# Optimization experiments

Measured on AMD Instinct MI355X. Metric: run time of the kernel, lower is better.

Reference implementation:

```python
import jax, jax.numpy as jnp
import numpy as np
import math

B, T, C = 4, 2048, 1024
N_HEAD = 16


def setup_inputs() -> dict:
    key = jax.random.key(0)
    k1, k2, k3 = jax.random.split(key, 3)
    x = jax.random.normal(k1, (B, T, C), dtype=jnp.float32)
    W_attn = jax.random.normal(k2, (C, 3 * C), dtype=jnp.float32) * (1.0 / math.sqrt(C))
    b_attn = jnp.zeros((3 * C,), dtype=jnp.float32)
    W_proj = jax.random.normal(k3, (C, C), dtype=jnp.float32) * (1.0 / math.sqrt(C))
    b_proj = jnp.zeros((C,), dtype=jnp.float32)
    return {"x": x, "W_attn": W_attn, "b_attn": b_attn, "W_proj": W_proj, "b_proj": b_proj}


def reference(x, W_attn, b_attn, W_proj, b_proj):
    b, t, c = x.shape
    hs = c // N_HEAD  # head size
    qkv = x @ W_attn + b_attn  # [B,T,3C]
    q, k, v = jnp.split(qkv, 3, axis=-1)
    # [B,T,C] -> [B,H,T,hs]
    q = q.reshape(b, t, N_HEAD, hs).transpose(0, 2, 1, 3)
    k = k.reshape(b, t, N_HEAD, hs).transpose(0, 2, 1, 3)
    v = v.reshape(b, t, N_HEAD, hs).transpose(0, 2, 1, 3)
    att = jnp.einsum('bhqd,bhkd->bhqk', q, k) / math.sqrt(hs)  # [B,H,T,T]
    causal = jnp.tril(jnp.ones((t, t), dtype=bool))
    att = jnp.where(causal[None, None, :, :], att, -jnp.inf)
    att = jax.nn.softmax(att, axis=-1)
    y = jnp.einsum('bhqk,bhkd->bhqd', att, v)  # [B,H,T,hs]
    y = y.transpose(0, 2, 1, 3).reshape(b, t, c)
    return y @ W_proj + b_proj
```

## Files before the change

### kernel.cpp

```cpp
#include <hip/hip_runtime.h>


typedef __bf16 bf16_t;
typedef __bf16 bf16x8 __attribute__((ext_vector_type(8)));
typedef __bf16 bf16x4 __attribute__((ext_vector_type(4)));
typedef float  f32x4  __attribute__((ext_vector_type(4)));

#define MFMA16(a, b, c) __builtin_amdgcn_mfma_f32_16x16x32_bf16((a), (b), (c), 0, 0, 0)

static __device__ __forceinline__ void gld_lds16(const bf16_t* g, void* l) {
  __builtin_amdgcn_global_load_lds(
      (const __attribute__((address_space(1))) void*)(const void*)g,
      (__attribute__((address_space(3))) void*)l, 16, 0, 0);
}

static __device__ __forceinline__ bf16x8 ldv8(const void* p) {
  return *reinterpret_cast<const bf16x8*>(p);
}

static __device__ __forceinline__ float exp2_hw(float x) {
  float r;
  asm("v_exp_f32 %0, %1" : "=v"(r) : "v"(x));
  return r;
}

__global__ __launch_bounds__(256) void cvt_f32_bf16(const float* __restrict__ in,
                                                    bf16_t* __restrict__ out, int n4) {
  int i = blockIdx.x * 256 + threadIdx.x;
  if (i < n4) {
    float4 v = reinterpret_cast<const float4*>(in)[i];
    bf16x4 o;
    o[0] = (bf16_t)v.x; o[1] = (bf16_t)v.y; o[2] = (bf16_t)v.z; o[3] = (bf16_t)v.w;
    reinterpret_cast<bf16x4*>(out)[i] = o;
  }
}

__global__ __launch_bounds__(256) void transpose_cvt(const float* __restrict__ in,
                                                     bf16_t* __restrict__ out,
                                                     int Kd, int Nd) {
  __shared__ float tile[32][33];
  int tx = threadIdx.x, ty = threadIdx.y;
  int n0 = blockIdx.x * 32, k0 = blockIdx.y * 32;
#pragma unroll
  for (int i = 0; i < 4; ++i)
    tile[ty + i * 8][tx] = in[(size_t)(k0 + ty + i * 8) * Nd + (n0 + tx)];
  __syncthreads();
#pragma unroll
  for (int i = 0; i < 4; ++i)
    out[(size_t)(n0 + ty + i * 8) * Kd + (k0 + tx)] = (bf16_t)tile[tx][ty + i * 8];
}

template <int MODE>
__global__ __launch_bounds__(256) void gemm_bf16(
    const bf16_t* __restrict__ A, const bf16_t* __restrict__ Bt,
    const float* __restrict__ bias, int M, int N, int K,
    bf16_t* __restrict__ Qo, bf16_t* __restrict__ Ko, bf16_t* __restrict__ Vt,
    float* __restrict__ Co) {
  __shared__ alignas(16) char lds[32768];

  const int tid = threadIdx.x;
  const int wave = tid >> 6, lane = tid & 63;
  const int wm = wave >> 1, wn = wave & 1;
  const int l16 = lane & 15, kb = lane >> 4;

  const int nbx = gridDim.x;
  const int lb = blockIdx.y * nbx + blockIdx.x;
  const int c = lb & 7;
  const int ii = lb >> 3;
  const int rPer = gridDim.y >> 3;
  const int tmt = c * rPer + (ii % rPer);
  const int tnt = ii / rPer;
  const int tm0 = tmt * 128, tn0 = tnt * 128;

  const int srow = wave * 8 + (lane >> 3);
  const int sp = lane & 7;

  f32x4 acc[4][4] = {};

  for (int k0 = 0; k0 < K; k0 += 64) {
    __syncthreads();
#pragma unroll
    for (int inst = 0; inst < 4; ++inst) {
      const int row = inst * 32 + srow;
      const int chunk = (sp ^ (row & 7)) * 8;
      gld_lds16(A + (size_t)(tm0 + row) * K + k0 + chunk,
                &lds[inst * 4096 + wave * 1024]);
      gld_lds16(Bt + (size_t)(tn0 + row) * K + k0 + chunk,
                &lds[16384 + inst * 4096 + wave * 1024]);
    }
    __syncthreads();
#pragma unroll
    for (int kc = 0; kc < 2; ++kc) {
      bf16x8 af[4], bfr[4];
#pragma unroll
      for (int mi = 0; mi < 4; ++mi) {
        const int row = wm * 64 + mi * 16 + l16;
        const int slot = (kc * 4 + kb) ^ (row & 7);
        af[mi] = ldv8(&lds[row * 128 + slot * 16]);
      }
#pragma unroll
      for (int ni = 0; ni < 4; ++ni) {
        const int row = wn * 64 + ni * 16 + l16;
        const int slot = (kc * 4 + kb) ^ (row & 7);
        bfr[ni] = ldv8(&lds[16384 + row * 128 + slot * 16]);
      }
#pragma unroll
      for (int mi = 0; mi < 4; ++mi)
#pragma unroll
        for (int ni = 0; ni < 4; ++ni)
          acc[mi][ni] = MFMA16(af[mi], bfr[ni], acc[mi][ni]);
    }
  }

#pragma unroll
  for (int ni = 0; ni < 4; ++ni) {
    const int n = tn0 + wn * 64 + ni * 16 + l16;
    const float bv = bias[n];
#pragma unroll
    for (int mi = 0; mi < 4; ++mi) {
#pragma unroll
      for (int j = 0; j < 4; ++j) {
        const int m = tm0 + wm * 64 + mi * 16 + kb * 4 + j;
        const float v = acc[mi][ni][j] + bv;
        if constexpr (MODE == 0) {
          const int which = n >> 10, hn = n & 1023;
          const int h = hn >> 6, d = hn & 63;
          const int b = m >> 11, t = m & 2047;
          const size_t bh = (size_t)(b * 16 + h);
          if (which == 0)
            Qo[(bh * 2048 + t) * 64 + d] = (bf16_t)(v * 0.18033688011112042f);
          else if (which == 1)
            Ko[(bh * 2048 + t) * 64 + d] = (bf16_t)v;
          else
            Vt[(bh * 64 + d) * 2048 + t] = (bf16_t)v;
        } else {
          Co[(size_t)m * N + n] = v;
        }
      }
    }
  }
}

__global__ __launch_bounds__(256) void attn_fwd(const bf16_t* __restrict__ Qg,
                                                const bf16_t* __restrict__ Kg,
                                                const bf16_t* __restrict__ Vtg,
                                                bf16_t* __restrict__ Yg) {
  __shared__ alignas(16) char lds[40960];

  const int tid = threadIdx.x;
  const int wave = tid >> 6, lane = tid & 63;
  const int l16 = lane & 15, kb = lane >> 4;
  const int l8 = l16 & 7;
  const float NEG_INF = -__builtin_inff();

  const int n = blockIdx.x;
  const int bh = (n & 7) * 8 + ((n >> 3) & 7);
  const int qt = 31 - (n >> 6);
  const size_t base = (size_t)bh * (2048 * 64);
  const int b = bh >> 4, h = bh & 15;

  const int srow = tid >> 3;
  const int schunk = (tid & 7) ^ (srow & 7);
  const bf16_t* Ksrc = Kg + base + (size_t)srow * 64 + schunk * 8;
  const bf16_t* Vsrc = Vtg + base + (size_t)srow * 2048 + schunk * 8;

  auto stageK = [&](int buf, int kv0) {
    char* kd = lds + buf * 8192 + wave * 1024;
    const bf16_t* ks = Ksrc + (size_t)kv0 * 64;
    gld_lds16(ks, kd);
    gld_lds16(ks + 2048, kd + 4096);
  };
  auto stageV = [&](int buf, int kv0) {
    char* vd = lds + 16384 + buf * 8192 + wave * 1024;
    const bf16_t* vs = Vsrc + kv0;
    gld_lds16(vs, vd);
    gld_lds16(vs + 65536, vd + 4096);
  };

  const int q0 = qt * 64 + wave * 16;
  const int q = q0 + l16;
  const int trips = qt + 1;

  const bf16x8 qf0 = ldv8(Qg + base + (size_t)q * 64 + kb * 8);
  const bf16x8 qf1 = ldv8(Qg + base + (size_t)q * 64 + 32 + kb * 8);

  f32x4 o[4] = {};
  float m_r = NEG_INF, l_r = 0.f;

  char* Pw = lds + 32768 + wave * 2048;

  stageK(0, 0);
  stageV(0, 0);
  asm volatile("s_waitcnt vmcnt(0)" ::: "memory");
  __builtin_amdgcn_s_barrier();
  __builtin_amdgcn_sched_barrier(0);

  int cur = 0;
  for (int t = 0; t < trips; ++t) {
    const int kv0 = t * 64;
    const bool more = (t + 1 < trips);
    if (more) {
      stageK(cur ^ 1, kv0 + 64);
      stageV(cur ^ 1, kv0 + 64);
    }

    const char* Kb = lds + cur * 8192;
    const char* Vb = lds + 16384 + cur * 8192;

    bf16x8 kf[8];
#pragma unroll
    for (int i = 0; i < 4; ++i) {
      const int row = i * 16 + l16;
#pragma unroll
      for (int kc = 0; kc < 2; ++kc)
        kf[i * 2 + kc] = ldv8(Kb + row * 128 + (((kc * 4 + kb) ^ (row & 7)) * 16));
    }

    f32x4 s[4] = {};
    __builtin_amdgcn_s_setprio(1);
#pragma unroll
    for (int i = 0; i < 4; ++i) {
      s[i] = MFMA16(kf[i * 2 + 0], qf0, s[i]);
      s[i] = MFMA16(kf[i * 2 + 1], qf1, s[i]);
    }
    __builtin_amdgcn_s_setprio(0);

    bf16x8 vf[8];
#pragma unroll
    for (int i = 0; i < 4; ++i) {
      const int row = i * 16 + l16;
#pragma unroll
      for (int kc = 0; kc < 2; ++kc)
        vf[i * 2 + kc] = ldv8(Vb + row * 128 + (((kc * 4 + kb) ^ (row & 7)) * 16));
    }

    float pm[4];
    if (t == qt) {
#pragma unroll
      for (int i = 0; i < 4; ++i) {
        f32x4 sv = s[i];
#pragma unroll
        for (int j = 0; j < 4; ++j)
          if (kv0 + i * 16 + kb * 4 + j > q) sv[j] = NEG_INF;
        s[i] = sv;
        pm[i] = fmaxf(fmaxf(sv[0], sv[1]), fmaxf(sv[2], sv[3]));
      }
    } else {
#pragma unroll
      for (int i = 0; i < 4; ++i)
        pm[i] = fmaxf(fmaxf(s[i][0], s[i][1]), fmaxf(s[i][2], s[i][3]));
    }
    float mx = fmaxf(fmaxf(pm[0], pm[1]), fmaxf(pm[2], pm[3]));
    if (__any(mx > m_r + 8.0f)) {
      mx = fmaxf(mx, __shfl_xor(mx, 16));
      mx = fmaxf(mx, __shfl_xor(mx, 32));
      const float mn = fmaxf(m_r, mx);
      const float sc = exp2_hw(m_r - mn);
      l_r *= sc;
#pragma unroll
      for (int i = 0; i < 4; ++i) {
        o[i][0] *= sc; o[i][1] *= sc; o[i][2] *= sc; o[i][3] *= sc;
      }
      m_r = mn;
    }
    float ss = 0.f;
    bf16x4 pw[4];
#pragma unroll
    for (int i = 0; i < 4; ++i)
#pragma unroll
      for (int j = 0; j < 4; ++j) {
        const float p = exp2_hw(s[i][j] - m_r);
        ss += p;
        pw[i][j] = (bf16_t)p;
      }
    l_r += ss;

#pragma unroll
    for (int i = 0; i < 4; ++i) {
      const int phys = (i * 2 + (kb >> 1)) ^ l8;
      *reinterpret_cast<bf16x4*>(Pw + l16 * 128 + phys * 16 + (kb & 1) * 8) = pw[i];
    }
    const bf16x8 pb0 = ldv8(Pw + l16 * 128 + ((kb ^ l8) * 16));
    const bf16x8 pb1 = ldv8(Pw + l16 * 128 + (((4 + kb) ^ l8) * 16));

    __builtin_amdgcn_s_setprio(1);
#pragma unroll
    for (int i = 0; i < 4; ++i) {
      o[i] = MFMA16(vf[i * 2 + 0], pb0, o[i]);
      o[i] = MFMA16(vf[i * 2 + 1], pb1, o[i]);
    }
    __builtin_amdgcn_s_setprio(0);

    asm volatile("s_waitcnt vmcnt(0)" ::: "memory");
    __builtin_amdgcn_s_barrier();
    __builtin_amdgcn_sched_barrier(0);
    cur ^= 1;
  }

  float lt = l_r + __shfl_xor(l_r, 16);
  lt += __shfl_xor(lt, 32);
  const float inv = 1.0f / lt;
  bf16_t* yrow = Yg + ((size_t)(b * 2048 + q)) * 1024 + h * 64;
#pragma unroll
  for (int i = 0; i < 4; ++i) {
    bf16x4 yv;
    yv[0] = (bf16_t)(o[i][0] * inv);
    yv[1] = (bf16_t)(o[i][1] * inv);
    yv[2] = (bf16_t)(o[i][2] * inv);
    yv[3] = (bf16_t)(o[i][3] * inv);
    *reinterpret_cast<bf16x4*>(yrow + i * 16 + kb * 4) = yv;
  }
}

extern "C" void kernel_launch(void* const* d_in, const int* in_sizes, int n_in,
                              void* d_out, int out_size, void* d_ws, size_t ws_size,
                              hipStream_t stream) {
  const float* x = (const float*)d_in[0];
  const float* W_attn = (const float*)d_in[1];
  const float* b_attn = (const float*)d_in[2];
  const float* W_proj = (const float*)d_in[3];
  const float* b_proj = (const float*)d_in[4];
  float* out = (float*)d_out;

  char* ws = (char*)d_ws;
  bf16_t* xb  = (bf16_t*)(ws + 0);
  bf16_t* WaT = (bf16_t*)(ws + 16777216);
  bf16_t* WpT = (bf16_t*)(ws + 23068672);
  bf16_t* Qb  = (bf16_t*)(ws + 25165824);
  bf16_t* Kb  = (bf16_t*)(ws + 41943040);
  bf16_t* Vt  = (bf16_t*)(ws + 58720256);
  bf16_t* Yb  = (bf16_t*)(ws + 75497472);

  cvt_f32_bf16<<<8192, 256, 0, stream>>>(x, xb, 8192 * 1024 / 4);
  transpose_cvt<<<dim3(96, 32), dim3(32, 8), 0, stream>>>(W_attn, WaT, 1024, 3072);
  transpose_cvt<<<dim3(32, 32), dim3(32, 8), 0, stream>>>(W_proj, WpT, 1024, 1024);

  gemm_bf16<0><<<dim3(24, 64), 256, 0, stream>>>(xb, WaT, b_attn, 8192, 3072, 1024,
                                                 Qb, Kb, Vt, nullptr);

  attn_fwd<<<2048, 256, 0, stream>>>(Qb, Kb, Vt, Yb);

  gemm_bf16<1><<<dim3(8, 64), 256, 0, stream>>>(Yb, WpT, b_proj, 8192, 1024, 1024,
                                                nullptr, nullptr, nullptr, out);
}
```

Measured before the change: 182.7 us.

## Rewrite GEMMs as 8-wave 256x128 tiles with triple-buffered LDS pipeline

Replaces the 4-wave 128x128 GEMM with a 512-thread kernel computing 256x128 tiles. K-tiles are triple-buffered in LDS and loaded asynchronously through global_load_lds, with A and B prefetch split across two half-steps and paced by explicit vmcnt waits, barriers and setprio around the MFMA bursts. The goal is to hide global-load latency and raise MFMA utilization in the QKV and output projections. In exchange it uses 144KB of LDS per block, limiting occupancy to one block per CU, and relies on hand-tuned waitcnt counts being correct.

```diff
diff --git a/kernel.cpp b/kernel.cpp
--- a/kernel.cpp
+++ b/kernel.cpp
@@ -51,17 +51,18 @@
 }
 
 template <int MODE>
-__global__ __launch_bounds__(256) void gemm_bf16(
+__global__ __launch_bounds__(512) void gemm8p(
     const bf16_t* __restrict__ A, const bf16_t* __restrict__ Bt,
     const float* __restrict__ bias, int M, int N, int K,
     bf16_t* __restrict__ Qo, bf16_t* __restrict__ Ko, bf16_t* __restrict__ Vt,
     float* __restrict__ Co) {
-  __shared__ alignas(16) char lds[32768];
+  __shared__ alignas(16) char lds[147456];
 
   const int tid = threadIdx.x;
   const int wave = tid >> 6, lane = tid & 63;
-  const int wm = wave >> 1, wn = wave & 1;
+  const int wm = wave >> 2, wn = wave & 3;
   const int l16 = lane & 15, kb = lane >> 4;
+  const int r7 = l16 & 7;
 
   const int nbx = gridDim.x;
   const int lb = blockIdx.y * nbx + blockIdx.x;
@@ -70,58 +71,109 @@
   const int rPer = gridDim.y >> 3;
   const int tmt = c * rPer + (ii % rPer);
   const int tnt = ii / rPer;
-  const int tm0 = tmt * 128, tn0 = tnt * 128;
-
-  const int srow = wave * 8 + (lane >> 3);
-  const int sp = lane & 7;
-
-  f32x4 acc[4][4] = {};
-
-  for (int k0 = 0; k0 < K; k0 += 64) {
-    __syncthreads();
-#pragma unroll
-    for (int inst = 0; inst < 4; ++inst) {
-      const int row = inst * 32 + srow;
-      const int chunk = (sp ^ (row & 7)) * 8;
-      gld_lds16(A + (size_t)(tm0 + row) * K + k0 + chunk,
-                &lds[inst * 4096 + wave * 1024]);
-      gld_lds16(Bt + (size_t)(tn0 + row) * K + k0 + chunk,
-                &lds[16384 + inst * 4096 + wave * 1024]);
-    }
-    __syncthreads();
-#pragma unroll
-    for (int kc = 0; kc < 2; ++kc) {
-      bf16x8 af[4], bfr[4];
-#pragma unroll
-      for (int mi = 0; mi < 4; ++mi) {
-        const int row = wm * 64 + mi * 16 + l16;
-        const int slot = (kc * 4 + kb) ^ (row & 7);
-        af[mi] = ldv8(&lds[row * 128 + slot * 16]);
-      }
-#pragma unroll
-      for (int ni = 0; ni < 4; ++ni) {
-        const int row = wn * 64 + ni * 16 + l16;
-        const int slot = (kc * 4 + kb) ^ (row & 7);
-        bfr[ni] = ldv8(&lds[16384 + row * 128 + slot * 16]);
-      }
-#pragma unroll
-      for (int mi = 0; mi < 4; ++mi)
-#pragma unroll
-        for (int ni = 0; ni < 4; ++ni)
-          acc[mi][ni] = MFMA16(af[mi], bfr[ni], acc[mi][ni]);
-    }
-  }
-
-#pragma unroll
-  for (int ni = 0; ni < 4; ++ni) {
-    const int n = tn0 + wn * 64 + ni * 16 + l16;
+  const int tm0 = tmt * 256, tn0 = tnt * 128;
+
+  const int srow = tid >> 3;
+  const int sch = (tid & 7) ^ (srow & 7);
+  const bf16_t* aR = A + (size_t)(tm0 + srow) * K + sch * 8;
+  const bf16_t* bR = Bt + (size_t)(tn0 + srow) * K + sch * 8;
+
+  auto stageA = [&](int buf, int kt) {
+    char* d = lds + buf * 49152 + wave * 1024;
+    const bf16_t* s = aR + kt * 64;
+#pragma unroll
+    for (int i = 0; i < 4; ++i)
+      gld_lds16(s + (size_t)(i * 64) * K, d + i * 8192);
+  };
+  auto stageB = [&](int buf, int kt) {
+    char* d = lds + buf * 49152 + 32768 + wave * 1024;
+    const bf16_t* s = bR + kt * 64;
+#pragma unroll
+    for (int i = 0; i < 2; ++i)
+      gld_lds16(s + (size_t)(i * 64) * K, d + i * 8192);
+  };
+
+  f32x4 acc[8][2] = {};
+  const int NK = K >> 6;
+
+  stageA(0, 0); stageB(0, 0);
+  stageA(1, 1); stageB(1, 1);
+  asm volatile("s_waitcnt vmcnt(6)" ::: "memory");
+  __builtin_amdgcn_s_barrier();
+  __builtin_amdgcn_sched_barrier(0);
+
+  for (int kt = 0; kt < NK; ++kt) {
+    const int buf = kt % 3;
+    const char* Ab = lds + buf * 49152;
+    const char* Bb = Ab + 32768;
+    const int nkt = kt + 2;
+    const int arow = wm * 128 + l16;
+    const int brow = wn * 32 + l16;
+
+    {
+      bf16x8 af[8], bfr[2];
+#pragma unroll
+      for (int m = 0; m < 8; ++m)
+        af[m] = ldv8(Ab + (arow + m * 16) * 128 + ((kb ^ r7) * 16));
+#pragma unroll
+      for (int nq = 0; nq < 2; ++nq)
+        bfr[nq] = ldv8(Bb + (brow + nq * 16) * 128 + ((kb ^ r7) * 16));
+      if (nkt < NK) stageA(nkt % 3, nkt);
+      __builtin_amdgcn_s_barrier();
+      asm volatile("s_waitcnt lgkmcnt(0)" ::: "memory");
+      __builtin_amdgcn_sched_barrier(0);
+      __builtin_amdgcn_s_setprio(1);
+#pragma unroll
+      for (int m = 0; m < 8; ++m) {
+        acc[m][0] = MFMA16(af[m], bfr[0], acc[m][0]);
+        acc[m][1] = MFMA16(af[m], bfr[1], acc[m][1]);
+      }
+      __builtin_amdgcn_s_setprio(0);
+      __builtin_amdgcn_s_barrier();
+      __builtin_amdgcn_sched_barrier(0);
+    }
+
+    {
+      bf16x8 af[8], bfr[2];
+#pragma unroll
+      for (int m = 0; m < 8; ++m)
+        af[m] = ldv8(Ab + (arow + m * 16) * 128 + (((4 + kb) ^ r7) * 16));
+#pragma unroll
+      for (int nq = 0; nq < 2; ++nq)
+        bfr[nq] = ldv8(Bb + (brow + nq * 16) * 128 + (((4 + kb) ^ r7) * 16));
+      if (nkt < NK) stageB(nkt % 3, nkt);
+      __builtin_amdgcn_s_barrier();
+      asm volatile("s_waitcnt lgkmcnt(0)" ::: "memory");
+      __builtin_amdgcn_sched_barrier(0);
+      __builtin_amdgcn_s_setprio(1);
+#pragma unroll
+      for (int m = 0; m < 8; ++m) {
+        acc[m][0] = MFMA16(af[m], bfr[0], acc[m][0]);
+        acc[m][1] = MFMA16(af[m], bfr[1], acc[m][1]);
+      }
+      __builtin_amdgcn_s_setprio(0);
+      if (kt + 1 < NK) {
+        if (nkt < NK) {
+          asm volatile("s_waitcnt vmcnt(6)" ::: "memory");
+        } else {
+          asm volatile("s_waitcnt vmcnt(0)" ::: "memory");
+        }
+      }
+      __builtin_amdgcn_s_barrier();
+      __builtin_amdgcn_sched_barrier(0);
+    }
+  }
+
+#pragma unroll
+  for (int nq = 0; nq < 2; ++nq) {
+    const int n = tn0 + wn * 32 + nq * 16 + l16;
     const float bv = bias[n];
 #pragma unroll
-    for (int mi = 0; mi < 4; ++mi) {
+    for (int mi = 0; mi < 8; ++mi) {
 #pragma unroll
       for (int j = 0; j < 4; ++j) {
-        const int m = tm0 + wm * 64 + mi * 16 + kb * 4 + j;
-        const float v = acc[mi][ni][j] + bv;
+        const int m = tm0 + wm * 128 + mi * 16 + kb * 4 + j;
+        const float v = acc[mi][nq][j] + bv;
         if constexpr (MODE == 0) {
           const int which = n >> 10, hn = n & 1023;
           const int h = hn >> 6, d = hn & 63;
@@ -335,11 +387,11 @@
   transpose_cvt<<<dim3(96, 32), dim3(32, 8), 0, stream>>>(W_attn, WaT, 1024, 3072);
   transpose_cvt<<<dim3(32, 32), dim3(32, 8), 0, stream>>>(W_proj, WpT, 1024, 1024);
 
-  gemm_bf16<0><<<dim3(24, 64), 256, 0, stream>>>(xb, WaT, b_attn, 8192, 3072, 1024,
-                                                 Qb, Kb, Vt, nullptr);
+  gemm8p<0><<<dim3(24, 32), 512, 0, stream>>>(xb, WaT, b_attn, 8192, 3072, 1024,
+                                              Qb, Kb, Vt, nullptr);
 
   attn_fwd<<<2048, 256, 0, stream>>>(Qb, Kb, Vt, Yb);
 
-  gemm_bf16<1><<<dim3(8, 64), 256, 0, stream>>>(Yb, WpT, b_proj, 8192, 1024, 1024,
-                                                nullptr, nullptr, nullptr, out);
-}
+  gemm8p<1><<<dim3(8, 32), 512, 0, stream>>>(Yb, WpT, b_proj, 8192, 1024, 1024,
+                                             nullptr, nullptr, nullptr, out);
+}
```

Result: no change. 185.8 us (+1.7%).
